# Kernel tuning notes

Measured on AMD Instinct MI355X. Metric: run time of the kernel, lower is better.

Reference implementation:

```python
import jax, jax.numpy as jnp
import numpy as np

B, S, H = 4, 256, 768
E, R, D = 200, 200, 25
NUM_ENT_TYPES, NUM_REL_TYPES = 9, 5
MAX_ENT_LEN = 100


def _make_span_mask(key, b, n, s, max_len):
    k1, k2 = jax.random.split(key)
    start = jax.random.randint(k1, (b, n), 0, s - max_len)
    length = jax.random.randint(k2, (b, n), 1, max_len)
    pos = jnp.arange(s)[None, None, :]
    return ((pos >= start[..., None]) & (pos < (start + length)[..., None])).astype(jnp.int32)


def setup_inputs() -> dict:
    key = jax.random.key(0)
    ks = jax.random.split(key, 9)
    lhs = jax.random.normal(ks[0], (B, S, H), dtype=jnp.float32)
    entity_mask = _make_span_mask(ks[1], B, E, S, 30)          # [B,E,S], span length < MAX_ENT_LEN
    relations = jax.random.randint(ks[2], (B, R, 2), 0, E).astype(jnp.int32)
    relation_context_mask = _make_span_mask(ks[3], B, R, S, 30)  # [B,R,S]
    size_emb = jax.random.normal(ks[4], (MAX_ENT_LEN, D), dtype=jnp.float32) * 0.02
    span_w = jax.random.normal(ks[5], (NUM_ENT_TYPES, D + 2 * H), dtype=jnp.float32) * 0.02
    span_b = jax.random.normal(ks[6], (NUM_ENT_TYPES,), dtype=jnp.float32) * 0.02
    rel_w = jax.random.normal(ks[7], (NUM_REL_TYPES, 2 * D + 3 * H), dtype=jnp.float32) * 0.02
    rel_b = jax.random.normal(ks[8], (NUM_REL_TYPES,), dtype=jnp.float32) * 0.02
    return {"last_hidden_state": lhs, "entity_mask": entity_mask, "relations": relations,
            "relation_context_mask": relation_context_mask, "size_emb": size_emb,
            "span_w": span_w, "span_b": span_b, "rel_w": rel_w, "rel_b": rel_b}


def _masked_maxpool(lhs, mask):
    # lhs: [B,S,H], mask: [B,N,S] (0/1) -> [B,N,H]
    # Faithful to torch: broadcast multiply (zeros included in max), then max over S.
    masked = lhs[:, None, :, :] * mask[:, :, :, None].astype(lhs.dtype)  # [B,N,S,H]
    return masked.max(axis=2)


def reference(last_hidden_state, entity_mask, relations, relation_context_mask,
              size_emb, span_w, span_b, rel_w, rel_b):
    b = last_hidden_state.shape[0]
    # --- entity classification ---
    entity_size = size_emb[entity_mask.sum(axis=-1)]               # [B,E,D]
    entity = _masked_maxpool(last_hidden_state, entity_mask)       # [B,E,H]
    context = last_hidden_state[:, 0, :]                           # CLS pooling [B,H]
    ctx = jnp.broadcast_to(context[:, None, :], entity.shape)      # [B,E,H]
    entity_repr = jnp.concatenate([entity, ctx, entity_size], axis=-1)
    entity_logit = entity_repr @ span_w.T + span_b                 # [B,E,num_entity_types]
    # --- relation classification ---
    rel_ctx = _masked_maxpool(last_hidden_state, relation_context_mask)  # [B,R,H]
    bidx = jnp.arange(b)[:, None, None]
    pair = entity[bidx, relations]                                 # [B,R,2,H]
    pair = pair.reshape(b, relations.shape[1], -1)                 # [B,R,2H]
    pair_size = entity_size[bidx, relations].reshape(b, relations.shape[1], -1)  # [B,R,2D]
    relation_repr = jnp.concatenate([rel_ctx, pair, pair_size], axis=-1)
    relation_logit = relation_repr @ rel_w.T + rel_b               # [B,R,num_relation_types]
    return entity_logit, relation_logit
```

## Files before the change

### kernel.cpp

```cpp
#include <hip/hip_runtime.h>
#include <math.h>

#define Bb 4
#define Ss 256
#define Hh 768
#define Ee 200
#define Rr 200
#define Dd 25
#define NET 9
#define NRT 5
#define ENT_REPR (Dd + 2*Hh)
#define REL_REPR (2*Dd + 3*Hh)
#define TPB 192
#define H4 (Hh/4)


__device__ __forceinline__ float4 max4(float4 a, float4 b) {
    return make_float4(fmaxf(a.x, b.x), fmaxf(a.y, b.y),
                       fmaxf(a.z, b.z), fmaxf(a.w, b.w));
}

__device__ __forceinline__ void span_wave(int4 m, int lane,
                                          int& first, int& last, int& length)
{
    const int p = lane * 4;
    int cnt = (m.x != 0) + (m.y != 0) + (m.z != 0) + (m.w != 0);
    int fm = m.x ? p : (m.y ? p+1 : (m.z ? p+2 : (m.w ? p+3 : 1024)));
    int lm = m.w ? p+3 : (m.z ? p+2 : (m.y ? p+1 : (m.x ? p : -1)));
    #pragma unroll
    for (int o = 32; o > 0; o >>= 1) {
        cnt += __shfl_xor(cnt, o, 64);
        fm   = min(fm, __shfl_xor(fm, o, 64));
        lm   = max(lm, __shfl_xor(lm, o, 64));
    }
    first = fm; last = lm; length = cnt;
}

__device__ __forceinline__ float4 pool4b(const float4* __restrict__ lb4,
                                         int col, int first, int last)
{
    float4 acc = make_float4(0.f, 0.f, 0.f, 0.f);
    for (int s = first; s <= last; s += 4) {
        const int r1 = min(s + 1, last);
        const int r2 = min(s + 2, last);
        const int r3 = min(s + 3, last);
        const float4 v0 = lb4[(size_t)s  * H4 + col];
        const float4 v1 = lb4[(size_t)r1 * H4 + col];
        const float4 v2 = lb4[(size_t)r2 * H4 + col];
        const float4 v3 = lb4[(size_t)r3 * H4 + col];
        acc = max4(acc, max4(max4(v0, v1), max4(v2, v3)));
    }
    return acc;
}

__global__ __launch_bounds__(TPB) void spert_fused(
    const float4* __restrict__ lhs4,
    const int*   __restrict__ ent_mask,
    const int*   __restrict__ relations,
    const int*   __restrict__ rel_mask,
    const float* __restrict__ size_emb,
    const float* __restrict__ span_w,
    const float* __restrict__ span_b,
    const float* __restrict__ rel_w,
    const float* __restrict__ rel_b,
    float* __restrict__ ent_logit,
    float* __restrict__ rel_logit)
{
    const int tid  = threadIdx.x;
    const int wave = tid >> 6;
    const int lane = tid & 63;
    const int item = blockIdx.x >> 1;
    const int b    = item / Ee;
    const int j    = item % Ee;
    const float4* lb4 = lhs4 + (size_t)b * Ss * H4;

    __shared__ float s_part[3][NET];

    if ((blockIdx.x & 1) == 0) {
        const float4 cx = lb4[tid];

        const int4 m = ((const int4*)(ent_mask + (size_t)(b*Ee + j)*Ss))[lane];
        int first, last, length;
        span_wave(m, lane, first, last, length);

        const float4 v  = pool4b(lb4, tid, first, last);
        const float  sz = (tid < Dd) ? size_emb[length * Dd + tid] : 0.0f;

        float sums[NET];
        #pragma unroll
        for (int t = 0; t < NET; ++t) {
            const float* w  = span_w + (size_t)t * ENT_REPR;
            const float* wa = w + 4*tid;
            const float* wb = w + Hh + 4*tid;
            float s = v.x*wa[0]  + v.y*wa[1]  + v.z*wa[2]  + v.w*wa[3]
                    + cx.x*wb[0] + cx.y*wb[1] + cx.z*wb[2] + cx.w*wb[3];
            if (tid < Dd) s += sz * w[2*Hh + tid];
            sums[t] = s;
        }
        #pragma unroll
        for (int t = 0; t < NET; ++t) {
            float s = sums[t];
            #pragma unroll
            for (int o = 32; o > 0; o >>= 1) s += __shfl_xor(s, o, 64);
            if (lane == 0) s_part[wave][t] = s;
        }
        __syncthreads();
        if (tid < NET) {
            ent_logit[(size_t)(b*Ee + j)*NET + tid] =
                s_part[0][tid] + s_part[1][tid] + s_part[2][tid] + span_b[tid];
        }
    } else {
        const int2 ee = ((const int2*)relations)[(size_t)b*Rr + j];
        const int e1 = ee.x, e2 = ee.y;

        const int4 mc = ((const int4*)(rel_mask + (size_t)(b*Rr + j)*Ss))[lane];
        const int4 m1 = ((const int4*)(ent_mask + (size_t)(b*Ee + e1)*Ss))[lane];
        const int4 m2 = ((const int4*)(ent_mask + (size_t)(b*Ee + e2)*Ss))[lane];

        int fc, lc, nc, f1, l1, n1, f2, l2, n2;
        {
            const int p = lane * 4;
            int c0 = (mc.x!=0)+(mc.y!=0)+(mc.z!=0)+(mc.w!=0);
            int c1 = (m1.x!=0)+(m1.y!=0)+(m1.z!=0)+(m1.w!=0);
            int c2 = (m2.x!=0)+(m2.y!=0)+(m2.z!=0)+(m2.w!=0);
            int F0 = mc.x?p:(mc.y?p+1:(mc.z?p+2:(mc.w?p+3:1024)));
            int F1 = m1.x?p:(m1.y?p+1:(m1.z?p+2:(m1.w?p+3:1024)));
            int F2 = m2.x?p:(m2.y?p+1:(m2.z?p+2:(m2.w?p+3:1024)));
            int L0 = mc.w?p+3:(mc.z?p+2:(mc.y?p+1:(mc.x?p:-1)));
            int L1 = m1.w?p+3:(m1.z?p+2:(m1.y?p+1:(m1.x?p:-1)));
            int L2 = m2.w?p+3:(m2.z?p+2:(m2.y?p+1:(m2.x?p:-1)));
            #pragma unroll
            for (int o = 32; o > 0; o >>= 1) {
                c0 += __shfl_xor(c0, o, 64);
                c1 += __shfl_xor(c1, o, 64);
                c2 += __shfl_xor(c2, o, 64);
                F0 = min(F0, __shfl_xor(F0, o, 64));
                F1 = min(F1, __shfl_xor(F1, o, 64));
                F2 = min(F2, __shfl_xor(F2, o, 64));
                L0 = max(L0, __shfl_xor(L0, o, 64));
                L1 = max(L1, __shfl_xor(L1, o, 64));
                L2 = max(L2, __shfl_xor(L2, o, 64));
            }
            fc = F0; lc = L0; nc = c0;
            f1 = F1; l1 = L1; n1 = c1;
            f2 = F2; l2 = L2; n2 = c2;
        }

        const float4 cx = pool4b(lb4, tid, fc, lc);
        const float4 a  = pool4b(lb4, tid, f1, l1);
        const float4 d  = pool4b(lb4, tid, f2, l2);
        const float sz1 = (tid < Dd) ? size_emb[n1 * Dd + tid] : 0.0f;
        const float sz2 = (tid < Dd) ? size_emb[n2 * Dd + tid] : 0.0f;

        float sums[NRT];
        #pragma unroll
        for (int t = 0; t < NRT; ++t) {
            const float* w  = rel_w + (size_t)t * REL_REPR;
            const float* wc = w + 4*tid;
            const float* wa = w + Hh + 4*tid;
            const float* wd = w + 2*Hh + 4*tid;
            float s = cx.x*wc[0] + cx.y*wc[1] + cx.z*wc[2] + cx.w*wc[3]
                    + a.x*wa[0]  + a.y*wa[1]  + a.z*wa[2]  + a.w*wa[3]
                    + d.x*wd[0]  + d.y*wd[1]  + d.z*wd[2]  + d.w*wd[3];
            if (tid < Dd) s += sz1 * w[3*Hh + tid] + sz2 * w[3*Hh + Dd + tid];
            sums[t] = s;
        }
        #pragma unroll
        for (int t = 0; t < NRT; ++t) {
            float s = sums[t];
            #pragma unroll
            for (int o = 32; o > 0; o >>= 1) s += __shfl_xor(s, o, 64);
            if (lane == 0) s_part[wave][t] = s;
        }
        __syncthreads();
        if (tid < NRT) {
            rel_logit[(size_t)(b*Rr + j)*NRT + tid] =
                s_part[0][tid] + s_part[1][tid] + s_part[2][tid] + rel_b[tid];
        }
    }
}

extern "C" void kernel_launch(void* const* d_in, const int* in_sizes, int n_in,
                              void* d_out, int out_size, void* d_ws, size_t ws_size,
                              hipStream_t stream) {
    const float* lhs       = (const float*)d_in[0];
    const int*   ent_mask  = (const int*)  d_in[1];
    const int*   relations = (const int*)  d_in[2];
    const int*   rel_mask  = (const int*)  d_in[3];
    const float* size_emb  = (const float*)d_in[4];
    const float* span_w    = (const float*)d_in[5];
    const float* span_b    = (const float*)d_in[6];
    const float* rel_w     = (const float*)d_in[7];
    const float* rel_b     = (const float*)d_in[8];

    float* ent_logit = (float*)d_out;
    float* rel_logit = (float*)d_out + (size_t)Bb*Ee*NET;

    spert_fused<<<2 * Bb * Ee, TPB, 0, stream>>>(
        (const float4*)lhs, ent_mask, relations, rel_mask, size_emb,
        span_w, span_b, rel_w, rel_b, ent_logit, rel_logit);
}
```

Measured before the change: 86.80 us.

## Batch multiple entities/relations per block with shared-memory staged weights

Each block now processes 4 relations or 8 entities instead of one item. Classifier weights are staged into padded shared memory once per block and reused across all items. The max-pool loop interleaves four spans at once to raise memory-level parallelism. This cuts the number of blocks and repeats fewer weight reads, at the cost of more registers, lockstep pooling sized to the longest span in the group, and a scalar staging loop with integer divides.

```diff
diff --git a/kernel.cpp b/kernel.cpp
--- a/kernel.cpp
+++ b/kernel.cpp
@@ -9,15 +9,25 @@
 #define Dd 25
 #define NET 9
 #define NRT 5
-#define ENT_REPR (Dd + 2*Hh)
-#define REL_REPR (2*Dd + 3*Hh)
+#define ENT_REPR 1561
+#define REL_REPR 2354
+#define SPAD 1568
+#define RPAD 2368
 #define TPB 192
-#define H4 (Hh/4)
+#define H4 192
+#define KENT 8
+#define KREL 4
+#define NBLK_REL (Bb*Rr/KREL)
+#define NBLK_ENT (Bb*Ee/KENT)
+#define SMEM_BYTES ((NET*SPAD + KENT*3*NET) * 4)
 
 
 __device__ __forceinline__ float4 max4(float4 a, float4 b) {
     return make_float4(fmaxf(a.x, b.x), fmaxf(a.y, b.y),
                        fmaxf(a.z, b.z), fmaxf(a.w, b.w));
+}
+__device__ __forceinline__ float dot4(float4 a, float4 b) {
+    return a.x*b.x + a.y*b.y + a.z*b.z + a.w*b.w;
 }
 
 __device__ __forceinline__ void span_wave(int4 m, int lane,
@@ -36,21 +46,27 @@
     first = fm; last = lm; length = cnt;
 }
 
-__device__ __forceinline__ float4 pool4b(const float4* __restrict__ lb4,
-                                         int col, int first, int last)
+__device__ __forceinline__ void pool_quad(const float4* __restrict__ lb4,
+    int col, int f0, int l0, int f1, int l1, int f2, int l2, int f3, int l3,
+    float4& a0, float4& a1, float4& a2, float4& a3)
 {
-    float4 acc = make_float4(0.f, 0.f, 0.f, 0.f);
-    for (int s = first; s <= last; s += 4) {
-        const int r1 = min(s + 1, last);
-        const int r2 = min(s + 2, last);
-        const int r3 = min(s + 3, last);
-        const float4 v0 = lb4[(size_t)s  * H4 + col];
-        const float4 v1 = lb4[(size_t)r1 * H4 + col];
-        const float4 v2 = lb4[(size_t)r2 * H4 + col];
-        const float4 v3 = lb4[(size_t)r3 * H4 + col];
-        acc = max4(acc, max4(max4(v0, v1), max4(v2, v3)));
+    const float4 z = make_float4(0.f, 0.f, 0.f, 0.f);
+    a0 = a1 = a2 = a3 = z;
+    const int n = max(max(l0 - f0, l1 - f1), max(l2 - f2, l3 - f3));
+    for (int s = 0; s <= n; s += 2) {
+        const float4 v00 = lb4[(size_t)min(f0 + s,     l0) * H4 + col];
+        const float4 v01 = lb4[(size_t)min(f0 + s + 1, l0) * H4 + col];
+        const float4 v10 = lb4[(size_t)min(f1 + s,     l1) * H4 + col];
+        const float4 v11 = lb4[(size_t)min(f1 + s + 1, l1) * H4 + col];
+        const float4 v20 = lb4[(size_t)min(f2 + s,     l2) * H4 + col];
+        const float4 v21 = lb4[(size_t)min(f2 + s + 1, l2) * H4 + col];
+        const float4 v30 = lb4[(size_t)min(f3 + s,     l3) * H4 + col];
+        const float4 v31 = lb4[(size_t)min(f3 + s + 1, l3) * H4 + col];
+        a0 = max4(a0, max4(v00, v01));
+        a1 = max4(a1, max4(v10, v11));
+        a2 = max4(a2, max4(v20, v21));
+        a3 = max4(a3, max4(v30, v31));
     }
-    return acc;
 }
 
 __global__ __launch_bounds__(TPB) void spert_fused(
@@ -66,116 +82,184 @@
     float* __restrict__ ent_logit,
     float* __restrict__ rel_logit)
 {
+    extern __shared__ float smem[];
     const int tid  = threadIdx.x;
     const int wave = tid >> 6;
     const int lane = tid & 63;
-    const int item = blockIdx.x >> 1;
-    const int b    = item / Ee;
-    const int j    = item % Ee;
-    const float4* lb4 = lhs4 + (size_t)b * Ss * H4;
-
-    __shared__ float s_part[3][NET];
-
-    if ((blockIdx.x & 1) == 0) {
+
+    if (blockIdx.x < NBLK_REL) {
+        float* s_w    = smem;
+        float* s_part = smem + NRT * RPAD;
+
+        const int item0 = blockIdx.x * KREL;
+        const int b  = item0 / Rr;
+        const int r0 = item0 % Rr;
+        const float4* lb4 = lhs4 + (size_t)b * Ss * H4;
+
+        int2 ee[KREL];
+        #pragma unroll
+        for (int i = 0; i < KREL; ++i)
+            ee[i] = ((const int2*)relations)[(size_t)b*Rr + r0 + i];
+
+        int4 mc[KREL], m1[KREL], m2[KREL];
+        #pragma unroll
+        for (int i = 0; i < KREL; ++i) {
+            mc[i] = ((const int4*)(rel_mask + (size_t)(b*Rr + r0 + i)*Ss))[lane];
+            m1[i] = ((const int4*)(ent_mask + (size_t)(b*Ee + ee[i].x)*Ss))[lane];
+            m2[i] = ((const int4*)(ent_mask + (size_t)(b*Ee + ee[i].y)*Ss))[lane];
+        }
+        int fc[KREL], lc[KREL], nc[KREL];
+        int f1[KREL], l1[KREL], n1[KREL];
+        int f2[KREL], l2[KREL], n2[KREL];
+        #pragma unroll
+        for (int i = 0; i < KREL; ++i) {
+            span_wave(mc[i], lane, fc[i], lc[i], nc[i]);
+            span_wave(m1[i], lane, f1[i], l1[i], n1[i]);
+            span_wave(m2[i], lane, f2[i], l2[i], n2[i]);
+        }
+
+        float4 cp[KREL], ap[KREL], dp[KREL];
+        pool_quad(lb4, tid, fc[0], lc[0], fc[1], lc[1], fc[2], lc[2], fc[3], lc[3],
+                  cp[0], cp[1], cp[2], cp[3]);
+        pool_quad(lb4, tid, f1[0], l1[0], f1[1], l1[1], f1[2], l1[2], f1[3], l1[3],
+                  ap[0], ap[1], ap[2], ap[3]);
+        pool_quad(lb4, tid, f2[0], l2[0], f2[1], l2[1], f2[2], l2[2], f2[3], l2[3],
+                  dp[0], dp[1], dp[2], dp[3]);
+
+        float sz1[KREL], sz2[KREL];
+        #pragma unroll
+        for (int i = 0; i < KREL; ++i) {
+            sz1[i] = (tid < Dd) ? size_emb[n1[i] * Dd + tid] : 0.0f;
+            sz2[i] = (tid < Dd) ? size_emb[n2[i] * Dd + tid] : 0.0f;
+        }
+
+        {
+            const float4* src4 = (const float4*)rel_w;
+            for (int k4 = tid; k4 < (NRT * REL_REPR) / 4; k4 += TPB) {
+                const float4 v = src4[k4];
+                const float* ve = (const float*)&v;
+                #pragma unroll
+                for (int e = 0; e < 4; ++e) {
+                    const int kk = 4 * k4 + e;
+                    const int t  = kk / REL_REPR;
+                    s_w[t * RPAD + (kk - t * REL_REPR)] = ve[e];
+                }
+            }
+            if (tid < 2)
+                s_w[4 * RPAD + 2352 + tid] = rel_w[11768 + tid];
+        }
+        __syncthreads();
+
+        #pragma unroll
+        for (int t = 0; t < NRT; ++t) {
+            const float4* w4 = (const float4*)(s_w + t * RPAD);
+            const float4 wc = w4[tid];
+            const float4 wa = w4[192 + tid];
+            const float4 wd = w4[384 + tid];
+            const float w31 = (tid < Dd) ? s_w[t * RPAD + 3*Hh + tid] : 0.0f;
+            const float w32 = (tid < Dd) ? s_w[t * RPAD + 3*Hh + Dd + tid] : 0.0f;
+            float sm[KREL];
+            #pragma unroll
+            for (int i = 0; i < KREL; ++i)
+                sm[i] = dot4(cp[i], wc) + dot4(ap[i], wa) + dot4(dp[i], wd)
+                      + sz1[i] * w31 + sz2[i] * w32;
+            #pragma unroll
+            for (int o = 32; o > 0; o >>= 1) {
+                #pragma unroll
+                for (int i = 0; i < KREL; ++i)
+                    sm[i] += __shfl_xor(sm[i], o, 64);
+            }
+            if (lane == 0) {
+                #pragma unroll
+                for (int i = 0; i < KREL; ++i)
+                    s_part[(i * 3 + wave) * NRT + t] = sm[i];
+            }
+        }
+        __syncthreads();
+        if (tid < KREL * NRT) {
+            const int i = tid / NRT, t = tid % NRT;
+            rel_logit[(size_t)(b*Rr + r0 + i)*NRT + t] =
+                s_part[(i*3 + 0)*NRT + t] + s_part[(i*3 + 1)*NRT + t]
+              + s_part[(i*3 + 2)*NRT + t] + rel_b[t];
+        }
+    } else {
+        float* s_w    = smem;
+        float* s_part = smem + NET * SPAD;
+
+        const int bi    = blockIdx.x - NBLK_REL;
+        const int item0 = bi * KENT;
+        const int b  = item0 / Ee;
+        const int e0 = item0 % Ee;
+        const float4* lb4 = lhs4 + (size_t)b * Ss * H4;
+
         const float4 cx = lb4[tid];
 
-        const int4 m = ((const int4*)(ent_mask + (size_t)(b*Ee + j)*Ss))[lane];
-        int first, last, length;
-        span_wave(m, lane, first, last, length);
-
-        const float4 v  = pool4b(lb4, tid, first, last);
-        const float  sz = (tid < Dd) ? size_emb[length * Dd + tid] : 0.0f;
-
-        float sums[NET];
+        int4 mk[KENT];
+        #pragma unroll
+        for (int i = 0; i < KENT; ++i)
+            mk[i] = ((const int4*)(ent_mask + (size_t)(b*Ee + e0 + i)*Ss))[lane];
+        int fs[KENT], ls[KENT], ln[KENT];
+        #pragma unroll
+        for (int i = 0; i < KENT; ++i)
+            span_wave(mk[i], lane, fs[i], ls[i], ln[i]);
+
+        float4 vp[KENT];
+        pool_quad(lb4, tid, fs[0], ls[0], fs[1], ls[1], fs[2], ls[2], fs[3], ls[3],
+                  vp[0], vp[1], vp[2], vp[3]);
+        pool_quad(lb4, tid, fs[4], ls[4], fs[5], ls[5], fs[6], ls[6], fs[7], ls[7],
+                  vp[4], vp[5], vp[6], vp[7]);
+
+        float sz[KENT];
+        #pragma unroll
+        for (int i = 0; i < KENT; ++i)
+            sz[i] = (tid < Dd) ? size_emb[ln[i] * Dd + tid] : 0.0f;
+
+        {
+            const float4* src4 = (const float4*)span_w;
+            for (int k4 = tid; k4 < (NET * ENT_REPR) / 4; k4 += TPB) {
+                const float4 v = src4[k4];
+                const float* ve = (const float*)&v;
+                #pragma unroll
+                for (int e = 0; e < 4; ++e) {
+                    const int kk = 4 * k4 + e;
+                    const int t  = kk / ENT_REPR;
+                    s_w[t * SPAD + (kk - t * ENT_REPR)] = ve[e];
+                }
+            }
+            if (tid == 0)
+                s_w[8 * SPAD + 1560] = span_w[14048];
+        }
+        __syncthreads();
+
         #pragma unroll
         for (int t = 0; t < NET; ++t) {
-            const float* w  = span_w + (size_t)t * ENT_REPR;
-            const float* wa = w + 4*tid;
-            const float* wb = w + Hh + 4*tid;
-            float s = v.x*wa[0]  + v.y*wa[1]  + v.z*wa[2]  + v.w*wa[3]
-                    + cx.x*wb[0] + cx.y*wb[1] + cx.z*wb[2] + cx.w*wb[3];
-            if (tid < Dd) s += sz * w[2*Hh + tid];
-            sums[t] = s;
-        }
-        #pragma unroll
-        for (int t = 0; t < NET; ++t) {
-            float s = sums[t];
-            #pragma unroll
-            for (int o = 32; o > 0; o >>= 1) s += __shfl_xor(s, o, 64);
-            if (lane == 0) s_part[wave][t] = s;
-        }
-        __syncthreads();
-        if (tid < NET) {
-            ent_logit[(size_t)(b*Ee + j)*NET + tid] =
-                s_part[0][tid] + s_part[1][tid] + s_part[2][tid] + span_b[tid];
-        }
-    } else {
-        const int2 ee = ((const int2*)relations)[(size_t)b*Rr + j];
-        const int e1 = ee.x, e2 = ee.y;
-
-        const int4 mc = ((const int4*)(rel_mask + (size_t)(b*Rr + j)*Ss))[lane];
-        const int4 m1 = ((const int4*)(ent_mask + (size_t)(b*Ee + e1)*Ss))[lane];
-        const int4 m2 = ((const int4*)(ent_mask + (size_t)(b*Ee + e2)*Ss))[lane];
-
-        int fc, lc, nc, f1, l1, n1, f2, l2, n2;
-        {
-            const int p = lane * 4;
-            int c0 = (mc.x!=0)+(mc.y!=0)+(mc.z!=0)+(mc.w!=0);
-            int c1 = (m1.x!=0)+(m1.y!=0)+(m1.z!=0)+(m1.w!=0);
-            int c2 = (m2.x!=0)+(m2.y!=0)+(m2.z!=0)+(m2.w!=0);
-            int F0 = mc.x?p:(mc.y?p+1:(mc.z?p+2:(mc.w?p+3:1024)));
-            int F1 = m1.x?p:(m1.y?p+1:(m1.z?p+2:(m1.w?p+3:1024)));
-            int F2 = m2.x?p:(m2.y?p+1:(m2.z?p+2:(m2.w?p+3:1024)));
-            int L0 = mc.w?p+3:(mc.z?p+2:(mc.y?p+1:(mc.x?p:-1)));
-            int L1 = m1.w?p+3:(m1.z?p+2:(m1.y?p+1:(m1.x?p:-1)));
-            int L2 = m2.w?p+3:(m2.z?p+2:(m2.y?p+1:(m2.x?p:-1)));
+            const float4* w4 = (const float4*)(s_w + t * SPAD);
+            const float4 wa = w4[tid];
+            const float4 wb = w4[192 + tid];
+            const float w2 = (tid < Dd) ? s_w[t * SPAD + 2*Hh + tid] : 0.0f;
+            const float base = dot4(cx, wb);
+            float sm[KENT];
+            #pragma unroll
+            for (int i = 0; i < KENT; ++i)
+                sm[i] = dot4(vp[i], wa) + base + sz[i] * w2;
             #pragma unroll
             for (int o = 32; o > 0; o >>= 1) {
-                c0 += __shfl_xor(c0, o, 64);
-                c1 += __shfl_xor(c1, o, 64);
-                c2 += __shfl_xor(c2, o, 64);
-                F0 = min(F0, __shfl_xor(F0, o, 64));
-                F1 = min(F1, __shfl_xor(F1, o, 64));
-                F2 = min(F2, __shfl_xor(F2, o, 64));
-                L0 = max(L0, __shfl_xor(L0, o, 64));
-                L1 = max(L1, __shfl_xor(L1, o, 64));
-                L2 = max(L2, __shfl_xor(L2, o, 64));
-            }
-            fc = F0; lc = L0; nc = c0;
-            f1 = F1; l1 = L1; n1 = c1;
-            f2 = F2; l2 = L2; n2 = c2;
-        }
-
-        const float4 cx = pool4b(lb4, tid, fc, lc);
-        const float4 a  = pool4b(lb4, tid, f1, l1);
-        const float4 d  = pool4b(lb4, tid, f2, l2);
-        const float sz1 = (tid < Dd) ? size_emb[n1 * Dd + tid] : 0.0f;
-        const float sz2 = (tid < Dd) ? size_emb[n2 * Dd + tid] : 0.0f;
-
-        float sums[NRT];
-        #pragma unroll
-        for (int t = 0; t < NRT; ++t) {
-            const float* w  = rel_w + (size_t)t * REL_REPR;
-            const float* wc = w + 4*tid;
-            const float* wa = w + Hh + 4*tid;
-            const float* wd = w + 2*Hh + 4*tid;
-            float s = cx.x*wc[0] + cx.y*wc[1] + cx.z*wc[2] + cx.w*wc[3]
-                    + a.x*wa[0]  + a.y*wa[1]  + a.z*wa[2]  + a.w*wa[3]
-                    + d.x*wd[0]  + d.y*wd[1]  + d.z*wd[2]  + d.w*wd[3];
-            if (tid < Dd) s += sz1 * w[3*Hh + tid] + sz2 * w[3*Hh + Dd + tid];
-            sums[t] = s;
-        }
-        #pragma unroll
-        for (int t = 0; t < NRT; ++t) {
-            float s = sums[t];
-            #pragma unroll
-            for (int o = 32; o > 0; o >>= 1) s += __shfl_xor(s, o, 64);
-            if (lane == 0) s_part[wave][t] = s;
-        }
-        __syncthreads();
-        if (tid < NRT) {
-            rel_logit[(size_t)(b*Rr + j)*NRT + tid] =
-                s_part[0][tid] + s_part[1][tid] + s_part[2][tid] + rel_b[tid];
+                #pragma unroll
+                for (int i = 0; i < KENT; ++i)
+                    sm[i] += __shfl_xor(sm[i], o, 64);
+            }
+            if (lane == 0) {
+                #pragma unroll
+                for (int i = 0; i < KENT; ++i)
+                    s_part[(i * 3 + wave) * NET + t] = sm[i];
+            }
+        }
+        __syncthreads();
+        if (tid < KENT * NET) {
+            const int i = tid / NET, t = tid % NET;
+            ent_logit[(size_t)(b*Ee + e0 + i)*NET + t] =
+                s_part[(i*3 + 0)*NET + t] + s_part[(i*3 + 1)*NET + t]
+              + s_part[(i*3 + 2)*NET + t] + span_b[t];
         }
     }
 }
@@ -196,7 +280,7 @@
     float* ent_logit = (float*)d_out;
     float* rel_logit = (float*)d_out + (size_t)Bb*Ee*NET;
 
-    spert_fused<<<2 * Bb * Ee, TPB, 0, stream>>>(
+    spert_fused<<<NBLK_REL + NBLK_ENT, TPB, SMEM_BYTES, stream>>>(
         (const float4*)lhs, ent_mask, relations, rel_mask, size_emb,
         span_w, span_b, rel_w, rel_b, ent_logit, rel_logit);
 }
```

After: 94.56 us. +8.9%, slower.
